# Kernel tuning notes

Measured on AMD Instinct MI355X. Metric: run time of the kernel, lower is better.

## Reference

```python
import jax, jax.numpy as jnp
import numpy as np

B, N, C, D, T = 16, 1024, 16, 64, 32  # batch, max_size, max_n_colors, inner_dim, timesteps


def setup_inputs() -> dict:
    key = jax.random.key(0)
    ks = jax.random.split(key, 16)
    s = 1.0 / np.sqrt(D)
    inp = {
        "Mvv": jax.random.randint(ks[0], (B, N, N), 0, 2).astype(jnp.float32),
        "n_colors": jax.random.randint(ks[1], (B,), 2, C + 1),
        # learned / initial states
        "v_init": jax.random.normal(ks[2], (D,)) * s,            # Normal(0,1)/sqrt(D)
        "ch0": jax.random.uniform(ks[3], (B, C, D)),             # Uniform(0,1) color init
        # recurrent GNN weights (simple tanh message-passing RNN)
        "W_v": jax.random.normal(ks[4], (D, D)) * s,
        "W_vv": jax.random.normal(ks[5], (D, D)) * s,
        "W_vc": jax.random.normal(ks[6], (D, D)) * s,
        "b_v": jnp.zeros((D,)),
        "W_c": jax.random.normal(ks[7], (D, D)) * s,
        "W_cv": jax.random.normal(ks[8], (D, D)) * s,
        "b_c": jnp.zeros((D,)),
        # vote MLP: Linear(D, D//4) -> Sigmoid -> Linear(D//4, 1)
        "W1": jax.random.normal(ks[9], (D, D // 4)) * s,
        "b1": jnp.zeros((D // 4,)),
        "W2": jax.random.normal(ks[10], (D // 4, 1)) * (1.0 / np.sqrt(D // 4)),
        "b2": jnp.zeros((1,)),
    }
    return inp


def reference(Mvv, n_colors, v_init, ch0, W_v, W_vv, W_vc, b_v, W_c, W_cv, b_c, W1, b1, W2, b2):
    # add self loops (Mvv += eye)
    A = Mvv + jnp.eye(N, dtype=Mvv.dtype)[None]
    # vectorized Mvc: Mvc[b, i, j] = 1 if j < n_colors[b]
    Mvc = jnp.broadcast_to(
        (jnp.arange(C)[None, None, :] < n_colors[:, None, None]).astype(Mvv.dtype),
        (B, N, C),
    )
    # hidden state init: v_init repeated over batch/nodes
    vh0 = jnp.broadcast_to(v_init, (B, N, D))

    def step(carry, _):
        vh, ch = carry
        v_agg = jnp.einsum("bnm,bmd->bnd", A, vh)      # neighbor aggregation
        c_agg = jnp.einsum("bnc,bcd->bnd", Mvc, ch)    # color -> vertex messages
        vh_new = jnp.tanh(vh @ W_v + v_agg @ W_vv + c_agg @ W_vc + b_v)
        cv_agg = jnp.einsum("bnc,bnd->bcd", Mvc, vh_new)  # vertex -> color messages
        ch_new = jnp.tanh(ch @ W_c + cv_agg @ W_cv + b_c)
        return (vh_new, ch_new), None

    (vh, _), _ = jax.lax.scan(step, (vh0, ch0), None, length=T)

    # vote MLP + mean over nodes + sigmoid
    vote = jax.nn.sigmoid(vh @ W1 + b1) @ W2 + b2      # [B, N, 1]
    pred = jax.nn.sigmoid(jnp.mean(vote, axis=1)).squeeze()  # [B]
    return pred
```

## Files before the change

kernel.cpp:

```cpp
#include <hip/hip_runtime.h>
#include <hip/hip_bf16.h>
#include <math.h>

#define BB 16
#define NN 1024
#define CC 16
#define DD 64
#define TT 32

typedef __bf16 bf16;
typedef __bf16 bf16x8 __attribute__((ext_vector_type(8)));
typedef __bf16 bf16x4 __attribute__((ext_vector_type(4)));
typedef float f32x4 __attribute__((ext_vector_type(4)));
typedef unsigned int u32;
typedef unsigned long long u64;
typedef u32 u32v4 __attribute__((ext_vector_type(4)));

__device__ __forceinline__ void split2(float x, bf16& h, bf16& l) {
    h = (bf16)x;
    l = (bf16)(x - (float)h);
}

__device__ __forceinline__ bf16x8 expand_bits(u32 b8) {
    u32 w[4];
    #pragma unroll
    for (int p = 0; p < 4; ++p) {
        u32 tt = b8 >> (2 * p);
        w[p] = ((tt & 1u) | ((tt & 2u) << 15)) * 0x3F80u;
    }
    u32v4 u = { w[0], w[1], w[2], w[3] };
    return __builtin_bit_cast(bf16x8, u);
}


__global__ __launch_bounds__(256) void prep_kernel(
    const float* __restrict__ Mvv, const float* __restrict__ v_init,
    const float* __restrict__ W_v, const float* __restrict__ W_vv,
    u64* __restrict__ Abits,
    bf16* __restrict__ vhHi, bf16* __restrict__ vhLo,
    bf16* __restrict__ VfHi, bf16* __restrict__ VfLo,
    bf16* __restrict__ WvTh, bf16* __restrict__ WvTl,
    bf16* __restrict__ WvvTh, bf16* __restrict__ WvvTl)
{
    int gid = blockIdx.x, tid = threadIdx.x;
    if (gid < 4096) {
        int w = tid >> 6, lane = tid & 63;
        for (int it = 0; it < 16; ++it) {
            int W = gid * 64 + w * 16 + it;
            int bb  = W >> 14;
            int row = (W >> 4) & 1023;
            int wq  = W & 15;
            float x = Mvv[(((size_t)bb << 10) + row) * 1024 + wq * 64 + lane];
            u64 m = __ballot(x != 0.0f);
            if (lane == 0) Abits[W] = m;
        }
    } else if (gid < 4608) {
        size_t idx = ((size_t)(gid - 4096) * 256 + tid) * 8;
        int d0 = (int)(idx & (DD - 1));
        bf16x8 oh, ol;
        #pragma unroll
        for (int e = 0; e < 8; ++e) { bf16 h, l; split2(v_init[d0 + e], h, l); oh[e] = h; ol[e] = l; }
        *(bf16x8*)(vhHi + idx) = oh;
        *(bf16x8*)(vhLo + idx) = ol;
    } else if (gid < 5120) {
        size_t idx = ((size_t)(gid - 4608) * 256 + tid) * 8;
        int j = (int)((idx >> 5) & 63);
        bf16 h, l; split2(v_init[j], h, l);
        bf16x8 oh, ol;
        #pragma unroll
        for (int e = 0; e < 8; ++e) { oh[e] = h; ol[e] = l; }
        *(bf16x8*)(VfHi + idx) = oh;
        *(bf16x8*)(VfLo + idx) = ol;
    } else {
        for (int e = tid; e < DD * DD; e += 256) {
            int n = e >> 6, k = e & 63;
            bf16 h, l;
            split2(W_v[k * DD + n], h, l);
            WvTh[e] = h; WvTl[e] = l;
            split2(W_vv[k * DD + n], h, l);
            WvvTh[e] = h; WvvTl[e] = l;
        }
    }
}

__global__ __launch_bounds__(512, 2) void step_kernel(
    const u64* __restrict__ Abits,
    const bf16* __restrict__ vhHi_in, const bf16* __restrict__ vhLo_in,
    const bf16* __restrict__ VfHi_in, const bf16* __restrict__ VfLo_in,
    bf16* __restrict__ vhHi_out, bf16* __restrict__ vhLo_out,
    bf16* __restrict__ VfHi_out, bf16* __restrict__ VfLo_out,
    const float* __restrict__ ch_in, float* __restrict__ ch_out,
    const float* __restrict__ part_prev, float* __restrict__ part_out,
    const int* __restrict__ n_colors,
    const float* __restrict__ Wc, const float* __restrict__ Wcv, const float* __restrict__ bc,
    const float* __restrict__ Wvc, const float* __restrict__ bv,
    const bf16* __restrict__ WvTh, const bf16* __restrict__ WvTl,
    const bf16* __restrict__ WvvTh, const bf16* __restrict__ WvvTl,
    int t)
{
    __shared__ float sWc[4096], sWcv[4096], sWvc[4096];
    __shared__ float sChI[1024], sChN[1024], sPart[4096];
    __shared__ float sRed[512];
    __shared__ float sBc[64], sBv[64], sVs[64], sMv[64], sCs[64], sCv[64];
    __shared__ float vagg[2][64 * 65];

    int tid  = threadIdx.x;
    int b    = blockIdx.x & 15;
    int blkr = blockIdx.x >> 4;
    int m0   = blkr * 64;
    int ncol = n_colors[b];
    int d = tid & 63, q = tid >> 6;

    for (int e = tid; e < 4096; e += 512) { sWvc[e] = Wvc[e]; sWc[e] = Wc[e]; sWcv[e] = Wcv[e]; }
    for (int e = tid; e < 1024; e += 512) sChI[e] = ch_in[(size_t)b * 1024 + e];
    if (t > 0)
        for (int e = tid; e < 4096; e += 512) sPart[e] = part_prev[(size_t)b * 4096 + e];
    if (tid < 64) { sBc[tid] = bc[tid]; sBv[tid] = bv[tid]; }

    int lane = tid & 63, w = tid >> 6;
    int l16 = lane & 15, lhi = lane >> 4;
    int wm = w & 1, wn = (w >> 1) & 1, wk = w >> 2;

    f32x4 acc[2][2];
    #pragma unroll
    for (int mi = 0; mi < 2; ++mi)
        #pragma unroll
        for (int nt = 0; nt < 2; ++nt) acc[mi][nt] = (f32x4){0.f, 0.f, 0.f, 0.f};

    const u64* Ab = Abits + ((size_t)b * NN + m0 + wm * 32 + l16) * 16 + wk * 8;
    const bf16* VfH = VfHi_in + (size_t)b * 65536;
    const bf16* VfL = VfLo_in + (size_t)b * 65536;

    #pragma unroll
    for (int kt = 0; kt < 4; ++kt) {
        u32v4 aw0 = *(const u32v4*)(Ab + kt * 2);
        u32v4 aw1 = *(const u32v4*)(Ab + 256 + kt * 2);
        #pragma unroll
        for (int kk = 0; kk < 4; ++kk) {
            int ks = wk * 16 + kt * 4 + kk;
            bf16x8 a0 = expand_bits((aw0[kk] >> (lhi * 8)) & 0xFFu);
            bf16x8 a1 = expand_bits((aw1[kk] >> (lhi * 8)) & 0xFFu);
            size_t fo = (size_t)ks * 2048 + (wn * 32 + l16) * 32 + lhi * 8;
            bf16x8 bh0 = *(const bf16x8*)(VfH + fo);
            bf16x8 bl0 = *(const bf16x8*)(VfL + fo);
            bf16x8 bh1 = *(const bf16x8*)(VfH + fo + 512);
            bf16x8 bl1 = *(const bf16x8*)(VfL + fo + 512);
            acc[0][0] = __builtin_amdgcn_mfma_f32_16x16x32_bf16(a0, bh0, acc[0][0], 0, 0, 0);
            acc[0][1] = __builtin_amdgcn_mfma_f32_16x16x32_bf16(a0, bh1, acc[0][1], 0, 0, 0);
            acc[1][0] = __builtin_amdgcn_mfma_f32_16x16x32_bf16(a1, bh0, acc[1][0], 0, 0, 0);
            acc[1][1] = __builtin_amdgcn_mfma_f32_16x16x32_bf16(a1, bh1, acc[1][1], 0, 0, 0);
            acc[0][0] = __builtin_amdgcn_mfma_f32_16x16x32_bf16(a0, bl0, acc[0][0], 0, 0, 0);
            acc[0][1] = __builtin_amdgcn_mfma_f32_16x16x32_bf16(a0, bl1, acc[0][1], 0, 0, 0);
            acc[1][0] = __builtin_amdgcn_mfma_f32_16x16x32_bf16(a1, bl0, acc[1][0], 0, 0, 0);
            acc[1][1] = __builtin_amdgcn_mfma_f32_16x16x32_bf16(a1, bl1, acc[1][1], 0, 0, 0);
        }
    }

    #pragma unroll
    for (int mi = 0; mi < 2; ++mi)
        #pragma unroll
        for (int nt = 0; nt < 2; ++nt)
            #pragma unroll
            for (int r = 0; r < 4; ++r)
                vagg[wk][(wm * 32 + mi * 16 + lhi * 4 + r) * 65 + wn * 32 + nt * 16 + l16] = acc[mi][nt][r];

    __syncthreads();

    if (t > 0) {
        {
            float s = 0.f;
            #pragma unroll
            for (int j = 0; j < 8; ++j) s += sPart[(q * 8 + j) * 64 + d];
            sRed[tid] = s;
        }
        __syncthreads();
        if (tid < 64) {
            float v = 0.f;
            #pragma unroll
            for (int i = 0; i < 8; ++i) v += sRed[tid + 64 * i];
            sVs[tid] = v;
        }
        __syncthreads();
        {
            float pm = 0.f;
            #pragma unroll
            for (int j = 0; j < 8; ++j) { int k = q * 8 + j; pm += sVs[k] * sWcv[k * 64 + d]; }
            sRed[tid] = pm;
        }
        __syncthreads();
        if (tid < 64) {
            float v = 0.f;
            #pragma unroll
            for (int i = 0; i < 8; ++i) v += sRed[tid + 64 * i];
            sMv[tid] = v;
        }
        __syncthreads();
        #pragma unroll
        for (int ci = 0; ci < 2; ++ci) {
            int c = q * 2 + ci;
            float s = sBc[d] + ((c < ncol) ? sMv[d] : 0.f);
            for (int k = 0; k < 64; ++k) s += sChI[c * 64 + k] * sWc[k * 64 + d];
            float cn = tanhf(s);
            sChN[c * 64 + d] = cn;
            ch_out[(size_t)b * 1024 + c * 64 + d] = cn;
        }
        __syncthreads();
        {
            float pcs = 0.f;
            #pragma unroll
            for (int ci = 0; ci < 2; ++ci) { int c = q * 2 + ci; if (c < ncol) pcs += sChN[c * 64 + d]; }
            sRed[tid] = pcs;
        }
        __syncthreads();
        if (tid < 64) {
            float v = 0.f;
            #pragma unroll
            for (int i = 0; i < 8; ++i) v += sRed[tid + 64 * i];
            sCs[tid] = v;
        }
        __syncthreads();
    } else {
        {
            float pcs = 0.f;
            #pragma unroll
            for (int ci = 0; ci < 2; ++ci) { int c = q * 2 + ci; if (c < ncol) pcs += sChI[c * 64 + d]; }
            sRed[tid] = pcs;
        }
        __syncthreads();
        if (tid < 64) {
            float v = 0.f;
            #pragma unroll
            for (int i = 0; i < 8; ++i) v += sRed[tid + 64 * i];
            sCs[tid] = v;
        }
        __syncthreads();
    }
    {
        float pv = 0.f;
        #pragma unroll
        for (int j = 0; j < 8; ++j) { int k = q * 8 + j; pv += sCs[k] * sWvc[k * 64 + d]; }
        sRed[tid] = pv;
    }
    __syncthreads();
    if (tid < 64) {
        float v = sBv[tid];
        #pragma unroll
        for (int i = 0; i < 8; ++i) v += sRed[tid + 64 * i];
        sCv[tid] = v;
    }
    __syncthreads();

    int rt = (w & 3) * 16, ct = (w >> 2) * 32;

    f32x4 p2[2][2];
    #pragma unroll
    for (int nt = 0; nt < 2; ++nt)
        #pragma unroll
        for (int kk = 0; kk < 2; ++kk) p2[nt][kk] = (f32x4){0.f, 0.f, 0.f, 0.f};

    #pragma unroll
    for (int kk = 0; kk < 2; ++kk) {
        int d0 = kk * 32 + lhi * 8;
        size_t vo = ((size_t)b * NN + m0 + rt + l16) * 64 + d0;
        bf16x8 a1h = *(const bf16x8*)(vhHi_in + vo);
        bf16x8 a1l = *(const bf16x8*)(vhLo_in + vo);
        int vb = (rt + l16) * 65 + d0;
        bf16x8 a2h, a2l;
        #pragma unroll
        for (int e = 0; e < 8; ++e) {
            float v = vagg[0][vb + e] + vagg[1][vb + e] + (float)a1h[e] + (float)a1l[e];
            bf16 h, l; split2(v, h, l);
            a2h[e] = h; a2l[e] = l;
        }
        #pragma unroll
        for (int nt = 0; nt < 2; ++nt) {
            int woff = (ct + nt * 16 + l16) * 64 + d0;
            bf16x8 b1h = *(const bf16x8*)(WvTh + woff);
            bf16x8 b1l = *(const bf16x8*)(WvTl + woff);
            bf16x8 b2h = *(const bf16x8*)(WvvTh + woff);
            bf16x8 b2l = *(const bf16x8*)(WvvTl + woff);
            p2[nt][kk] = __builtin_amdgcn_mfma_f32_16x16x32_bf16(a1h, b1h, p2[nt][kk], 0, 0, 0);
            p2[nt][kk] = __builtin_amdgcn_mfma_f32_16x16x32_bf16(a1l, b1h, p2[nt][kk], 0, 0, 0);
            p2[nt][kk] = __builtin_amdgcn_mfma_f32_16x16x32_bf16(a1h, b1l, p2[nt][kk], 0, 0, 0);
            p2[nt][kk] = __builtin_amdgcn_mfma_f32_16x16x32_bf16(a2h, b2h, p2[nt][kk], 0, 0, 0);
            p2[nt][kk] = __builtin_amdgcn_mfma_f32_16x16x32_bf16(a2l, b2h, p2[nt][kk], 0, 0, 0);
            p2[nt][kk] = __builtin_amdgcn_mfma_f32_16x16x32_bf16(a2h, b2l, p2[nt][kk], 0, 0, 0);
        }
    }

    int ksW = (m0 + rt) >> 5;
    int khi = 2 * ((rt >> 4) & 1) + (lhi >> 1);
    #pragma unroll
    for (int nt = 0; nt < 2; ++nt) {
        int col = ct + nt * 16 + l16;
        float cv = sCv[col];
        float tv[4];
        #pragma unroll
        for (int r = 0; r < 4; ++r) tv[r] = tanhf(p2[nt][0][r] + p2[nt][1][r] + cv);

        bf16x4 pkh, pkl;
        #pragma unroll
        for (int r = 0; r < 4; ++r) {
            bf16 h, l; split2(tv[r], h, l);
            size_t ro = ((size_t)b * NN + m0 + rt + lhi * 4 + r) * 64 + col;
            vhHi_out[ro] = h;
            vhLo_out[ro] = l;
            pkh[r] = h; pkl[r] = l;
        }
        size_t fo = (size_t)b * 65536 + (size_t)ksW * 2048 + col * 32 + khi * 8 + (lhi & 1) * 4;
        *(bf16x4*)(VfHi_out + fo) = pkh;
        *(bf16x4*)(VfLo_out + fo) = pkl;

        float cs = tv[0] + tv[1] + tv[2] + tv[3];
        cs += __shfl_xor(cs, 16);
        cs += __shfl_xor(cs, 32);
        if (lhi == 0)
            part_out[(((size_t)b * 16 + blkr) * 4 + (w & 3)) * 64 + col] = cs;
    }
}

__global__ __launch_bounds__(256) void final_part_kernel(
    const bf16* __restrict__ vhHi, const bf16* __restrict__ vhLo,
    const float* __restrict__ W1, const float* __restrict__ b1,
    const float* __restrict__ W2, float* __restrict__ partial)
{
    __shared__ float sX[64 * 65];
    __shared__ float sW1[1024];
    __shared__ float sb1v[16], sW2v[16];
    __shared__ float sRed[256];
    int tid = threadIdx.x;
    int b = blockIdx.x & 15, blk = blockIdx.x >> 4, n0 = blk * 64;

    for (int e = tid; e < 1024; e += 256) sW1[e] = W1[e];
    if (tid < 16) { sb1v[tid] = b1[tid]; sW2v[tid] = W2[tid]; }
    {
        const bf16* gh = vhHi + ((size_t)b * NN + n0) * DD;
        const bf16* gl = vhLo + ((size_t)b * NN + n0) * DD;
        #pragma unroll
        for (int u = 0; u < 2; ++u) {
            int e = tid + u * 256;
            bf16x8 h8 = *(const bf16x8*)(gh + e * 8);
            bf16x8 l8 = *(const bf16x8*)(gl + e * 8);
            int row = e >> 3;
            int col = (e & 7) * 8;
            #pragma unroll
            for (int k = 0; k < 8; ++k) sX[row * 65 + col + k] = (float)h8[k] + (float)l8[k];
        }
    }
    __syncthreads();

    int nl = tid & 63, q = tid >> 6;
    float h[4];
    #pragma unroll
    for (int j = 0; j < 4; ++j) h[j] = sb1v[q * 4 + j];
    for (int dd = 0; dd < 64; ++dd) {
        float x = sX[nl * 65 + dd];
        #pragma unroll
        for (int j = 0; j < 4; ++j) h[j] += x * sW1[dd * 16 + q * 4 + j];
    }
    float pv = 0.f;
    #pragma unroll
    for (int j = 0; j < 4; ++j) pv += sW2v[q * 4 + j] / (1.f + expf(-h[j]));
    sRed[tid] = pv;
    __syncthreads();
    if (tid < 64) {
        float vote = sRed[tid] + sRed[tid + 64] + sRed[tid + 128] + sRed[tid + 192];
        #pragma unroll
        for (int off = 1; off < 64; off <<= 1) vote += __shfl_xor(vote, off);
        if (tid == 0) partial[blockIdx.x] = vote;
    }
}

__global__ __launch_bounds__(256) void final_reduce_kernel(
    const float* __restrict__ partial, const float* __restrict__ b2, float* __restrict__ out)
{
    int tid = threadIdx.x;
    int b = tid >> 4, p = tid & 15;
    float v = partial[p * 16 + b];
    #pragma unroll
    for (int off = 1; off < 16; off <<= 1) v += __shfl_xor(v, off);
    if (p == 0) out[b] = 1.f / (1.f + expf(-(v / 1024.f + b2[0])));
}

extern "C" void kernel_launch(void* const* d_in, const int* in_sizes, int n_in,
                              void* d_out, int out_size, void* d_ws, size_t ws_size,
                              hipStream_t stream) {
    const float* Mvv  = (const float*)d_in[0];
    const int*   ncol = (const int*)d_in[1];
    const float* vini = (const float*)d_in[2];
    const float* ch0  = (const float*)d_in[3];
    const float* W_v  = (const float*)d_in[4];
    const float* W_vv = (const float*)d_in[5];
    const float* W_vc = (const float*)d_in[6];
    const float* b_v  = (const float*)d_in[7];
    const float* W_c  = (const float*)d_in[8];
    const float* W_cv = (const float*)d_in[9];
    const float* b_c  = (const float*)d_in[10];
    const float* W1   = (const float*)d_in[11];
    const float* b1   = (const float*)d_in[12];
    const float* W2   = (const float*)d_in[13];
    const float* b2   = (const float*)d_in[14];

    char* base = (char*)d_ws;
    size_t off = 0;
    u64* Abits = (u64*)(base + off); off += (size_t)BB * NN * 16 * 8;
    const size_t SVH = (size_t)BB * NN * DD * 2;
    bf16* vhHi[2] = {(bf16*)(base + off), (bf16*)(base + off + SVH)}; off += 2 * SVH;
    bf16* vhLo[2] = {(bf16*)(base + off), (bf16*)(base + off + SVH)}; off += 2 * SVH;
    bf16* VfHi[2] = {(bf16*)(base + off), (bf16*)(base + off + SVH)}; off += 2 * SVH;
    bf16* VfLo[2] = {(bf16*)(base + off), (bf16*)(base + off + SVH)}; off += 2 * SVH;
    const size_t SCH = (size_t)BB * CC * DD * 4;
    float* chb[2] = {(float*)(base + off), (float*)(base + off + SCH)}; off += 2 * SCH;
    const size_t SPB = (size_t)BB * 64 * DD * 4;
    float* pb[2] = {(float*)(base + off), (float*)(base + off + SPB)}; off += 2 * SPB;
    bf16* WvTh  = (bf16*)(base + off); off += DD * DD * 2;
    bf16* WvTl  = (bf16*)(base + off); off += DD * DD * 2;
    bf16* WvvTh = (bf16*)(base + off); off += DD * DD * 2;
    bf16* WvvTl = (bf16*)(base + off); off += DD * DD * 2;
    float* partial = (float*)(base + off); off += 256 * 4;

    prep_kernel<<<5121, 256, 0, stream>>>(Mvv, vini, W_v, W_vv, Abits,
        vhHi[0], vhLo[0], VfHi[0], VfLo[0], WvTh, WvTl, WvvTh, WvvTl);

    for (int t = 0; t < TT; ++t) {
        const float* ch_in = (t <= 1) ? ch0 : chb[(t - 1) & 1];
        int i = t & 1, o = (t + 1) & 1;
        step_kernel<<<256, 512, 0, stream>>>(Abits,
            vhHi[i], vhLo[i], VfHi[i], VfLo[i],
            vhHi[o], vhLo[o], VfHi[o], VfLo[o],
            ch_in, chb[t & 1],
            pb[(t + 1) & 1], pb[t & 1],
            ncol, W_c, W_cv, b_c, W_vc, b_v,
            WvTh, WvTl, WvvTh, WvvTl, t);
    }

    final_part_kernel<<<256, 256, 0, stream>>>(vhHi[0], vhLo[0], W1, b1, W2, partial);
    final_reduce_kernel<<<1, 256, 0, stream>>>(partial, b2, (float*)d_out);
}
```

Before: 740.3 us.

## Fuse vote MLP into last step, shrink shared memory, use fast tanh

Folds the final vote-MLP partial-sum kernel into the last timestep of the step kernel, which also skips writing vh outputs on that step. Shared memory drops by removing the Wcv/Wvc/sPart/sChN arrays: partials go to registers, Wcv and Wvc are read straight from global, and the new ch values are written back into sChI. The two tanhf calls become an exp-based fast_tanh. This removes one launch, some global traffic and shared memory pressure, at the cost of slight numeric differences and uncached global weight reads.

```diff
diff --git a/kernel.cpp b/kernel.cpp
--- a/kernel.cpp
+++ b/kernel.cpp
@@ -19,6 +19,13 @@
 __device__ __forceinline__ void split2(float x, bf16& h, bf16& l) {
     h = (bf16)x;
     l = (bf16)(x - (float)h);
+}
+
+__device__ __forceinline__ float fast_tanh(float x) {
+    float ax = fabsf(x);
+    float e = __expf(-2.f * ax);
+    float t = 1.f - 2.f * e / (1.f + e);
+    return copysignf(t, x);
 }
 
 __device__ __forceinline__ bf16x8 expand_bits(u32 b8) {
@@ -96,10 +103,12 @@
     const float* __restrict__ Wvc, const float* __restrict__ bv,
     const bf16* __restrict__ WvTh, const bf16* __restrict__ WvTl,
     const bf16* __restrict__ WvvTh, const bf16* __restrict__ WvvTl,
+    const float* __restrict__ W1, const float* __restrict__ b1, const float* __restrict__ W2,
+    float* __restrict__ partial,
     int t)
 {
-    __shared__ float sWc[4096], sWcv[4096], sWvc[4096];
-    __shared__ float sChI[1024], sChN[1024], sPart[4096];
+    __shared__ float sWc[4096];
+    __shared__ float sChI[1024];
     __shared__ float sRed[512];
     __shared__ float sBc[64], sBv[64], sVs[64], sMv[64], sCs[64], sCv[64];
     __shared__ float vagg[2][64 * 65];
@@ -111,11 +120,16 @@
     int ncol = n_colors[b];
     int d = tid & 63, q = tid >> 6;
 
-    for (int e = tid; e < 4096; e += 512) { sWvc[e] = Wvc[e]; sWc[e] = Wc[e]; sWcv[e] = Wcv[e]; }
+    for (int e = tid; e < 4096; e += 512) sWc[e] = Wc[e];
     for (int e = tid; e < 1024; e += 512) sChI[e] = ch_in[(size_t)b * 1024 + e];
-    if (t > 0)
-        for (int e = tid; e < 4096; e += 512) sPart[e] = part_prev[(size_t)b * 4096 + e];
     if (tid < 64) { sBc[tid] = bc[tid]; sBv[tid] = bv[tid]; }
+
+    float pr[8];
+    if (t > 0) {
+        #pragma unroll
+        for (int j = 0; j < 8; ++j)
+            pr[j] = part_prev[(size_t)b * 4096 + (q * 8 + j) * 64 + d];
+    }
 
     int lane = tid & 63, w = tid >> 6;
     int l16 = lane & 15, lhi = lane >> 4;
@@ -163,14 +177,13 @@
             #pragma unroll
             for (int r = 0; r < 4; ++r)
                 vagg[wk][(wm * 32 + mi * 16 + lhi * 4 + r) * 65 + wn * 32 + nt * 16 + l16] = acc[mi][nt][r];
-
     __syncthreads();
 
     if (t > 0) {
         {
             float s = 0.f;
             #pragma unroll
-            for (int j = 0; j < 8; ++j) s += sPart[(q * 8 + j) * 64 + d];
+            for (int j = 0; j < 8; ++j) s += pr[j];
             sRed[tid] = s;
         }
         __syncthreads();
@@ -184,7 +197,7 @@
         {
             float pm = 0.f;
             #pragma unroll
-            for (int j = 0; j < 8; ++j) { int k = q * 8 + j; pm += sVs[k] * sWcv[k * 64 + d]; }
+            for (int j = 0; j < 8; ++j) { int k = q * 8 + j; pm += sVs[k] * Wcv[k * 64 + d]; }
             sRed[tid] = pm;
         }
         __syncthreads();
@@ -195,50 +208,41 @@
             sMv[tid] = v;
         }
         __syncthreads();
+        float cn[2];
         #pragma unroll
         for (int ci = 0; ci < 2; ++ci) {
             int c = q * 2 + ci;
             float s = sBc[d] + ((c < ncol) ? sMv[d] : 0.f);
             for (int k = 0; k < 64; ++k) s += sChI[c * 64 + k] * sWc[k * 64 + d];
-            float cn = tanhf(s);
-            sChN[c * 64 + d] = cn;
-            ch_out[(size_t)b * 1024 + c * 64 + d] = cn;
-        }
-        __syncthreads();
-        {
-            float pcs = 0.f;
-            #pragma unroll
-            for (int ci = 0; ci < 2; ++ci) { int c = q * 2 + ci; if (c < ncol) pcs += sChN[c * 64 + d]; }
-            sRed[tid] = pcs;
-        }
-        __syncthreads();
-        if (tid < 64) {
-            float v = 0.f;
-            #pragma unroll
-            for (int i = 0; i < 8; ++i) v += sRed[tid + 64 * i];
-            sCs[tid] = v;
-        }
-        __syncthreads();
-    } else {
-        {
-            float pcs = 0.f;
-            #pragma unroll
-            for (int ci = 0; ci < 2; ++ci) { int c = q * 2 + ci; if (c < ncol) pcs += sChI[c * 64 + d]; }
-            sRed[tid] = pcs;
-        }
-        __syncthreads();
-        if (tid < 64) {
-            float v = 0.f;
-            #pragma unroll
-            for (int i = 0; i < 8; ++i) v += sRed[tid + 64 * i];
-            sCs[tid] = v;
-        }
-        __syncthreads();
-    }
+            cn[ci] = fast_tanh(s);
+        }
+        __syncthreads();
+        #pragma unroll
+        for (int ci = 0; ci < 2; ++ci) {
+            int c = q * 2 + ci;
+            sChI[c * 64 + d] = cn[ci];
+            ch_out[(size_t)b * 1024 + c * 64 + d] = cn[ci];
+        }
+        __syncthreads();
+    }
+    {
+        float pcs = 0.f;
+        #pragma unroll
+        for (int ci = 0; ci < 2; ++ci) { int c = q * 2 + ci; if (c < ncol) pcs += sChI[c * 64 + d]; }
+        sRed[tid] = pcs;
+    }
+    __syncthreads();
+    if (tid < 64) {
+        float v = 0.f;
+        #pragma unroll
+        for (int i = 0; i < 8; ++i) v += sRed[tid + 64 * i];
+        sCs[tid] = v;
+    }
+    __syncthreads();
     {
         float pv = 0.f;
         #pragma unroll
-        for (int j = 0; j < 8; ++j) { int k = q * 8 + j; pv += sCs[k] * sWvc[k * 64 + d]; }
+        for (int j = 0; j < 8; ++j) { int k = q * 8 + j; pv += sCs[k] * Wvc[k * 64 + d]; }
         sRed[tid] = pv;
     }
     __syncthreads();
@@ -288,86 +292,74 @@
         }
     }
 
-    int ksW = (m0 + rt) >> 5;
-    int khi = 2 * ((rt >> 4) & 1) + (lhi >> 1);
+    float tvv[2][4];
     #pragma unroll
     for (int nt = 0; nt < 2; ++nt) {
-        int col = ct + nt * 16 + l16;
-        float cv = sCv[col];
-        float tv[4];
-        #pragma unroll
-        for (int r = 0; r < 4; ++r) tv[r] = tanhf(p2[nt][0][r] + p2[nt][1][r] + cv);
-
-        bf16x4 pkh, pkl;
-        #pragma unroll
-        for (int r = 0; r < 4; ++r) {
-            bf16 h, l; split2(tv[r], h, l);
-            size_t ro = ((size_t)b * NN + m0 + rt + lhi * 4 + r) * 64 + col;
-            vhHi_out[ro] = h;
-            vhLo_out[ro] = l;
-            pkh[r] = h; pkl[r] = l;
-        }
-        size_t fo = (size_t)b * 65536 + (size_t)ksW * 2048 + col * 32 + khi * 8 + (lhi & 1) * 4;
-        *(bf16x4*)(VfHi_out + fo) = pkh;
-        *(bf16x4*)(VfLo_out + fo) = pkl;
-
-        float cs = tv[0] + tv[1] + tv[2] + tv[3];
-        cs += __shfl_xor(cs, 16);
-        cs += __shfl_xor(cs, 32);
-        if (lhi == 0)
-            part_out[(((size_t)b * 16 + blkr) * 4 + (w & 3)) * 64 + col] = cs;
-    }
-}
-
-__global__ __launch_bounds__(256) void final_part_kernel(
-    const bf16* __restrict__ vhHi, const bf16* __restrict__ vhLo,
-    const float* __restrict__ W1, const float* __restrict__ b1,
-    const float* __restrict__ W2, float* __restrict__ partial)
-{
-    __shared__ float sX[64 * 65];
-    __shared__ float sW1[1024];
-    __shared__ float sb1v[16], sW2v[16];
-    __shared__ float sRed[256];
-    int tid = threadIdx.x;
-    int b = blockIdx.x & 15, blk = blockIdx.x >> 4, n0 = blk * 64;
-
-    for (int e = tid; e < 1024; e += 256) sW1[e] = W1[e];
-    if (tid < 16) { sb1v[tid] = b1[tid]; sW2v[tid] = W2[tid]; }
-    {
-        const bf16* gh = vhHi + ((size_t)b * NN + n0) * DD;
-        const bf16* gl = vhLo + ((size_t)b * NN + n0) * DD;
-        #pragma unroll
-        for (int u = 0; u < 2; ++u) {
-            int e = tid + u * 256;
-            bf16x8 h8 = *(const bf16x8*)(gh + e * 8);
-            bf16x8 l8 = *(const bf16x8*)(gl + e * 8);
-            int row = e >> 3;
-            int col = (e & 7) * 8;
-            #pragma unroll
-            for (int k = 0; k < 8; ++k) sX[row * 65 + col + k] = (float)h8[k] + (float)l8[k];
-        }
-    }
-    __syncthreads();
-
-    int nl = tid & 63, q = tid >> 6;
-    float h[4];
-    #pragma unroll
-    for (int j = 0; j < 4; ++j) h[j] = sb1v[q * 4 + j];
-    for (int dd = 0; dd < 64; ++dd) {
-        float x = sX[nl * 65 + dd];
-        #pragma unroll
-        for (int j = 0; j < 4; ++j) h[j] += x * sW1[dd * 16 + q * 4 + j];
-    }
-    float pv = 0.f;
-    #pragma unroll
-    for (int j = 0; j < 4; ++j) pv += sW2v[q * 4 + j] / (1.f + expf(-h[j]));
-    sRed[tid] = pv;
-    __syncthreads();
-    if (tid < 64) {
-        float vote = sRed[tid] + sRed[tid + 64] + sRed[tid + 128] + sRed[tid + 192];
-        #pragma unroll
-        for (int off = 1; off < 64; off <<= 1) vote += __shfl_xor(vote, off);
-        if (tid == 0) partial[blockIdx.x] = vote;
+        float cv = sCv[ct + nt * 16 + l16];
+        #pragma unroll
+        for (int r = 0; r < 4; ++r) tvv[nt][r] = fast_tanh(p2[nt][0][r] + p2[nt][1][r] + cv);
+    }
+
+    if (t < TT - 1) {
+        int ksW = (m0 + rt) >> 5;
+        int khi = 2 * ((rt >> 4) & 1) + (lhi >> 1);
+        size_t vout_base = (size_t)b * NN * DD;
+        #pragma unroll
+        for (int nt = 0; nt < 2; ++nt) {
+            int col = ct + nt * 16 + l16;
+            float cs = tvv[nt][0] + tvv[nt][1] + tvv[nt][2] + tvv[nt][3];
+            cs += __shfl_xor(cs, 16);
+            cs += __shfl_xor(cs, 32);
+            if (lhi == 0)
+                part_out[(((size_t)b * 16 + blkr) * 4 + (w & 3)) * 64 + col] = cs;
+
+            bf16x4 pkh, pkl;
+            #pragma unroll
+            for (int r = 0; r < 4; ++r) {
+                bf16 h, l; split2(tvv[nt][r], h, l);
+                pkh[r] = h; pkl[r] = l;
+                size_t ro = vout_base + (size_t)(m0 + rt + lhi * 4 + r) * 64 + col;
+                vhHi_out[ro] = h;
+                vhLo_out[ro] = l;
+            }
+            size_t fo = (size_t)b * 65536 + (size_t)ksW * 2048 + col * 32 + khi * 8 + (lhi & 1) * 4;
+            *(bf16x4*)(VfHi_out + fo) = pkh;
+            *(bf16x4*)(VfLo_out + fo) = pkl;
+        }
+    } else {
+        __syncthreads();
+        float* sX  = &vagg[0][0];
+        float* sW1 = &vagg[1][0];
+        #pragma unroll
+        for (int nt = 0; nt < 2; ++nt) {
+            int col = ct + nt * 16 + l16;
+            #pragma unroll
+            for (int r = 0; r < 4; ++r)
+                sX[(rt + lhi * 4 + r) * 65 + col] = tvv[nt][r];
+        }
+        for (int e = tid; e < 1024; e += 512) sW1[e] = W1[e];
+        if (tid < 16) { sVs[tid] = W2[tid]; sMv[tid] = b1[tid]; }
+        __syncthreads();
+
+        int nl = tid & 63;
+        int jq = tid >> 6;
+        float h0 = sMv[jq * 2], h1 = sMv[jq * 2 + 1];
+        for (int dd = 0; dd < 64; ++dd) {
+            float x = sX[nl * 65 + dd];
+            h0 += x * sW1[dd * 16 + jq * 2];
+            h1 += x * sW1[dd * 16 + jq * 2 + 1];
+        }
+        float pv = sVs[jq * 2] / (1.f + __expf(-h0)) + sVs[jq * 2 + 1] / (1.f + __expf(-h1));
+        sRed[tid] = pv;
+        __syncthreads();
+        if (tid < 64) {
+            float v = 0.f;
+            #pragma unroll
+            for (int i = 0; i < 8; ++i) v += sRed[tid + 64 * i];
+            #pragma unroll
+            for (int off = 1; off < 64; off <<= 1) v += __shfl_xor(v, off);
+            if (tid == 0) partial[blockIdx.x] = v;
+        }
     }
 }
 
@@ -431,9 +423,9 @@
             ch_in, chb[t & 1],
             pb[(t + 1) & 1], pb[t & 1],
             ncol, W_c, W_cv, b_c, W_vc, b_v,
-            WvTh, WvTl, WvvTh, WvvTl, t);
-    }
-
-    final_part_kernel<<<256, 256, 0, stream>>>(vhHi[0], vhLo[0], W1, b1, W2, partial);
+            WvTh, WvTl, WvvTh, WvvTl,
+            W1, b1, W2, partial, t);
+    }
+
     final_reduce_kernel<<<1, 256, 0, stream>>>(partial, b2, (float*)d_out);
 }
```

New measurement: 703.0 us. 1.05x faster.
